# Performance work log

Measured on AMD Instinct MI355X. Metric: run time of the kernel, lower is better.

Reference implementation:

```python
import jax, jax.numpy as jnp
import numpy as np

_SAMPLING_EPS = 1e-5
_NEG_INF = jnp.float32(-jnp.inf)


def setup_inputs() -> dict:
    key = jax.random.key(0)
    k0, k1, k2, k3, k4, k5 = jax.random.split(key, 6)
    T, B, D, V = 4096, 64, 2048, 128000
    hidden_states = jax.random.normal(k0, (T, D), jnp.float32)
    embedding = jax.random.normal(k1, (V, D), jnp.float32) * 0.02
    last_token_indices = jnp.sort(jax.random.randint(k2, (B,), 0, T)).astype(jnp.int64)
    temperatures = jax.random.uniform(k3, (B,), jnp.float32, 0.1, 1.5)
    top_ps = jax.random.uniform(k4, (B,), jnp.float32, 0.5, 1.0)
    top_ks = jax.random.randint(k5, (B,), 1, 1024).astype(jnp.int64)
    return {
        "hidden_states": hidden_states,
        "embedding": embedding,
        "last_token_indices": last_token_indices,
        "temperatures": temperatures,
        "top_ps": top_ps,
        "top_ks": top_ks,
    }


def reference(hidden_states, embedding, last_token_indices, temperatures, top_ps, top_ks):
    V = embedding.shape[0]
    # 1) prune: keep last token of each sequence -> [B, D]
    h = hidden_states[last_token_indices]
    # 2) logits = h @ E^T -> [B, V]
    logits = jnp.einsum("bd,vd->bv", h, embedding)
    # 3) temperature scaling (temp < eps treated as 1.0, greedy handled below)
    t = jnp.where(temperatures < _SAMPLING_EPS, 1.0, temperatures)
    logits = logits / t[:, None]
    # 4) batched top-k in sorted (descending) domain
    sorted_idx = jnp.argsort(-logits, axis=-1)                      # [B, V]
    sorted_logits = jnp.take_along_axis(logits, sorted_idx, axis=-1)
    k = jnp.clip(top_ks, 1, V)
    keep_topk = jnp.arange(V)[None, :] < k[:, None]                  # [B, V]
    sorted_logits = jnp.where(keep_topk, sorted_logits, _NEG_INF)
    # 5) top-p (nucleus) on top-k-filtered, sorted logits
    sorted_probs = jax.nn.softmax(sorted_logits, axis=-1)
    cum = jnp.cumsum(sorted_probs, axis=-1)
    mask_p = (cum > top_ps[:, None]) & (top_ps[:, None] < 1.0 - _SAMPLING_EPS)
    mask_p = mask_p.at[:, 0].set(False)  # always keep the top token
    sorted_logits = jnp.where(mask_p, _NEG_INF, sorted_logits)
    # 6) scatter back to original vocab order
    inv_idx = jnp.argsort(sorted_idx, axis=-1)
    final_logits = jnp.take_along_axis(sorted_logits, inv_idx, axis=-1)
    probs = jax.nn.softmax(final_logits, axis=-1)
    # 7) multinomial sampling via Gumbel-max trick (deterministic key)
    u = jax.random.uniform(jax.random.key(42), probs.shape, jnp.float32, 1e-20, 1.0)
    gumbel = -jnp.log(-jnp.log(u))
    sampled = jnp.argmax(final_logits + gumbel, axis=-1)
    # 8) greedy path when temperature ~ 0
    greedy = jnp.argmax(logits, axis=-1)
    token_ids = jnp.where(temperatures < _SAMPLING_EPS, greedy, sampled)
    # sanitize (clamp out-of-range to 0)
    token_ids = jnp.where((token_ids < 0) | (token_ids >= V), 0, token_ids)
    return token_ids.astype(jnp.int64), probs
```

## Files before the change

kernel.cpp:

```cpp
#include <hip/hip_runtime.h>
#include <hip/hip_bf16.h>
#include <math.h>

#define CAP 2048
#define PRNG_PARTITIONABLE 1

typedef __attribute__((ext_vector_type(8))) short bf16x8;
typedef __attribute__((ext_vector_type(4))) float f32x4;
typedef __attribute__((ext_vector_type(4))) unsigned int u32x4;

union B8U4 { u32x4 u; bf16x8 b; };

#define BARRIER_LDS { asm volatile("s_waitcnt lgkmcnt(0)" ::: "memory"); \
                      __builtin_amdgcn_sched_barrier(0);                  \
                      __builtin_amdgcn_s_barrier(); }

__device__ __forceinline__ unsigned int f2ord(float x) {
  unsigned int u = __float_as_uint(x);
  return (u & 0x80000000u) ? ~u : (u | 0x80000000u);
}

__device__ __forceinline__ unsigned int rotl_u32(unsigned int x, int r) {
  return (x << r) | (x >> (32 - r));
}

__device__ float gumbel_at(unsigned int flat, unsigned int half_n) {
  const unsigned int ks0 = 0u;
  const unsigned int ks1 = 42u;
  const unsigned int ks2 = 0x1BD11BDAu ^ ks0 ^ ks1;
  unsigned int x0, x1;
#if PRNG_PARTITIONABLE
  x0 = 0u;
  x1 = flat;
#else
  unsigned int cnt = (flat < half_n) ? flat : (flat - half_n);
  x0 = cnt; x1 = cnt + half_n;
#endif
  x0 += ks0; x1 += ks1;
#define TF_R(r) { x0 += x1; x1 = rotl_u32(x1, r); x1 ^= x0; }
  TF_R(13) TF_R(15) TF_R(26) TF_R(6)
  x0 += ks1; x1 += ks2 + 1u;
  TF_R(17) TF_R(29) TF_R(16) TF_R(24)
  x0 += ks2; x1 += ks0 + 2u;
  TF_R(13) TF_R(15) TF_R(26) TF_R(6)
  x0 += ks0; x1 += ks1 + 3u;
  TF_R(17) TF_R(29) TF_R(16) TF_R(24)
  x0 += ks1; x1 += ks2 + 4u;
  TF_R(13) TF_R(15) TF_R(26) TF_R(6)
  x0 += ks2; x1 += ks0 + 5u;
#undef TF_R
#if PRNG_PARTITIONABLE
  unsigned int bits = x0 ^ x1;
#else
  unsigned int bits = (flat < half_n) ? x0 : x1;
#endif
  float f = __uint_as_float(0x3f800000u | (bits >> 9)) - 1.0f;
  float u = fmaxf(1e-20f, f + 1e-20f);
  return -logf(-logf(u));
}

__device__ __forceinline__ unsigned short f32_to_bf16_rne(float x) {
  unsigned int u = __float_as_uint(x);
  unsigned int r = u + 0x7fffu + ((u >> 16) & 1u);
  return (unsigned short)(r >> 16);
}
__device__ __forceinline__ float bf16u_to_f32(unsigned short h) {
  return __uint_as_float(((unsigned int)h) << 16);
}

struct HL { unsigned int h, l; };
__device__ __forceinline__ HL cvt_pair(float a, float b) {
  float2 xf = make_float2(a, b);
  __hip_bfloat162 hh = __float22bfloat162_rn(xf);
  float2 hf = __bfloat1622float2(hh);
  __hip_bfloat162 ll = __float22bfloat162_rn(make_float2(a - hf.x, b - hf.y));
  HL r;
  __builtin_memcpy(&r.h, &hh, 4);
  __builtin_memcpy(&r.l, &ll, 4);
  return r;
}

__device__ __forceinline__ f32x4 mfma16(bf16x8 a, bf16x8 b, f32x4 c) {
  return __builtin_amdgcn_mfma_f32_16x16x32_bf16(a, b, c, 0, 0, 0);
}

__global__ void gather_split(const float* __restrict__ hidden, const int* __restrict__ lti,
                             unsigned short* __restrict__ Ah, unsigned short* __restrict__ Al,
                             int D) {
  int b = blockIdx.x;
  const float* src = hidden + (size_t)lti[b] * D;
  for (int i = threadIdx.x; i < D; i += blockDim.x) {
    float x = src[i];
    unsigned short h = f32_to_bf16_rne(x);
    float r = x - bf16u_to_f32(h);
    Ah[(size_t)b * D + i] = h;
    Al[(size_t)b * D + i] = f32_to_bf16_rne(r);
  }
}

#define BN 128
#define BK 64
__global__ __launch_bounds__(256) void gemm_mfma(
    const unsigned short* __restrict__ Ahg, const unsigned short* __restrict__ Alg,
    const float* __restrict__ E, float* __restrict__ outL, int D, int V) {
  __shared__ __align__(16) float BS[128 * 64];
  __shared__ __align__(16) unsigned short AhS[64 * 64];
  __shared__ __align__(16) unsigned short AlS[64 * 64];

  const int t = threadIdx.x;
  const int lane = t & 63;
  const int wv = t >> 6;
  const long n0 = (long)blockIdx.x * BN;
  const int am = t >> 2, ao = t & 3;

  f32x4 acc[4][2];
#pragma unroll
  for (int i = 0; i < 4; ++i)
#pragma unroll
    for (int j = 0; j < 2; ++j) acc[i][j] = (f32x4){0.f, 0.f, 0.f, 0.f};

  f32x4 bA[8], bB[8];
  bf16x8 aA[4], aB[4];

  auto LOAD = [&](f32x4* br, bf16x8* ar, int k0) {
#pragma unroll
    for (int q = 0; q < 4; ++q) {
      int gi = q * 256 + t, n = gi >> 3, o = gi & 7;
      const float* s = E + (size_t)(n0 + n) * D + k0 + o * 8;
      br[2 * q] = *(const f32x4*)s;
      br[2 * q + 1] = *(const f32x4*)(s + 4);
    }
    const unsigned short* ph = Ahg + (size_t)am * D + k0 + ao * 16;
    ar[0] = *(const bf16x8*)ph;
    ar[1] = *(const bf16x8*)(ph + 8);
    const unsigned short* pl = Alg + (size_t)am * D + k0 + ao * 16;
    ar[2] = *(const bf16x8*)pl;
    ar[3] = *(const bf16x8*)(pl + 8);
  };

  auto STAGE = [&](f32x4* br, bf16x8* ar) {
#pragma unroll
    for (int q = 0; q < 4; ++q) {
      int gi = q * 256 + t, n = gi >> 3, o = gi & 7;
      int pg0 = (2 * o) ^ (n & 7);
      int pg1 = (2 * o + 1) ^ (n & 7);
      *(f32x4*)&BS[n * 64 + pg0 * 4] = br[2 * q];
      *(f32x4*)&BS[n * 64 + pg1 * 4] = br[2 * q + 1];
    }
    int g0 = ao * 2;
    int off0 = am * 64 + ((g0 ^ (am & 7)) * 8);
    int off1 = am * 64 + (((g0 + 1) ^ (am & 7)) * 8);
    *(bf16x8*)&AhS[off0] = ar[0];
    *(bf16x8*)&AhS[off1] = ar[1];
    *(bf16x8*)&AlS[off0] = ar[2];
    *(bf16x8*)&AlS[off1] = ar[3];
  };

  auto COMPUTE = [&]() {
#pragma unroll
    for (int k32 = 0; k32 < 2; ++k32) {
      const int og = k32 * 4 + (lane >> 4);
      bf16x8 ah[4], al[4], bh[2], bl[2];
#pragma unroll
      for (int mf = 0; mf < 4; ++mf) {
        int r = mf * 16 + (lane & 15);
        int off = r * 64 + ((og ^ (r & 7)) * 8);
        ah[mf] = *(const bf16x8*)&AhS[off];
        al[mf] = *(const bf16x8*)&AlS[off];
      }
#pragma unroll
      for (int nf = 0; nf < 2; ++nf) {
        int n = wv * 32 + nf * 16 + (lane & 15);
        int pg0 = (2 * og) ^ (n & 7);
        int pg1 = (2 * og + 1) ^ (n & 7);
        f32x4 v0 = *(const f32x4*)&BS[n * 64 + pg0 * 4];
        f32x4 v1 = *(const f32x4*)&BS[n * 64 + pg1 * 4];
        HL p0 = cvt_pair(v0.x, v0.y);
        HL p1 = cvt_pair(v0.z, v0.w);
        HL p2 = cvt_pair(v1.x, v1.y);
        HL p3 = cvt_pair(v1.z, v1.w);
        B8U4 hb, lb;
        hb.u = (u32x4){p0.h, p1.h, p2.h, p3.h};
        lb.u = (u32x4){p0.l, p1.l, p2.l, p3.l};
        bh[nf] = hb.b;
        bl[nf] = lb.b;
      }
      __builtin_amdgcn_s_setprio(1);
#pragma unroll
      for (int mf = 0; mf < 4; ++mf)
#pragma unroll
        for (int nf = 0; nf < 2; ++nf) {
          acc[mf][nf] = mfma16(ah[mf], bh[nf], acc[mf][nf]);
          acc[mf][nf] = mfma16(ah[mf], bl[nf], acc[mf][nf]);
          acc[mf][nf] = mfma16(al[mf], bh[nf], acc[mf][nf]);
        }
      __builtin_amdgcn_s_setprio(0);
    }
  };

  LOAD(bA, aA, 0);
#pragma unroll 1
  for (int k0 = 0; k0 < D; k0 += 2 * BK) {
    if (k0 + BK < D) LOAD(bB, aB, k0 + BK);
    BARRIER_LDS;
    STAGE(bA, aA);
    BARRIER_LDS;
    COMPUTE();
    if (k0 + 2 * BK < D) LOAD(bA, aA, k0 + 2 * BK);
    BARRIER_LDS;
    STAGE(bB, aB);
    BARRIER_LDS;
    COMPUTE();
  }

#pragma unroll
  for (int mf = 0; mf < 4; ++mf)
#pragma unroll
    for (int nf = 0; nf < 2; ++nf) {
      long v = n0 + wv * 32 + nf * 16 + (lane & 15);
      int rbase = mf * 16 + ((lane >> 4) << 2);
#pragma unroll
      for (int reg = 0; reg < 4; ++reg)
        outL[(size_t)(rbase + reg) * V + v] = acc[mf][nf][reg];
    }
}

__global__ __launch_bounds__(256) void hist_k(
    const float* __restrict__ logits, unsigned int* __restrict__ ghist, int V) {
  const int b = blockIdx.x >> 3, c = blockIdx.x & 7;
  const int CH = V >> 3;
  const float* row = logits + (size_t)b * V;
  __shared__ unsigned int lh[4096];
  const int tid = threadIdx.x;
  for (int i = tid; i < 4096; i += 256) lh[i] = 0u;
  __syncthreads();
  const int base = c * CH;
  for (int i = base + tid * 4; i < base + CH; i += 1024) {
    f32x4 v = *(const f32x4*)(row + i);
    atomicAdd(&lh[f2ord(v.x) >> 20], 1u);
    atomicAdd(&lh[f2ord(v.y) >> 20], 1u);
    atomicAdd(&lh[f2ord(v.z) >> 20], 1u);
    atomicAdd(&lh[f2ord(v.w) >> 20], 1u);
  }
  __syncthreads();
  for (int i = tid; i < 4096; i += 256) {
    unsigned int s = lh[i];
    if (s) atomicAdd(&ghist[(size_t)b * 4096 + i], s);
  }
}

__global__ __launch_bounds__(1024) void thresh_k(
    const float* __restrict__ logits, const unsigned int* __restrict__ ghist,
    const int* __restrict__ top_ks, unsigned int* __restrict__ tau20, int V) {
  const int b = blockIdx.x, tid = threadIdx.x;
  __shared__ unsigned int h[4096];
  __shared__ unsigned int ts[1024];
  __shared__ unsigned int h2[256];
  __shared__ int s_bin, s_cntGT, s_found;

  for (int i = tid; i < 4096; i += 1024) h[i] = ghist[(size_t)b * 4096 + i];
  if (tid == 0) s_found = 0;
  __syncthreads();

  int k = top_ks[b];
  if (k < 1) k = 1;
  if (k > V) k = V;
  const unsigned int uk = (unsigned int)k;

  unsigned int s0 = h[4 * tid] + h[4 * tid + 1] + h[4 * tid + 2] + h[4 * tid + 3];
  ts[tid] = s0;
  __syncthreads();
  for (int off = 1; off < 1024; off <<= 1) {
    unsigned int v = ts[tid] + ((tid + off < 1024) ? ts[tid + off] : 0u);
    __syncthreads();
    ts[tid] = v;
    __syncthreads();
  }
  unsigned int above = ts[tid] - s0;
  if (above < uk && above + s0 >= uk) {
    unsigned int run = above;
    for (int j = 3; j >= 0; --j) {
      unsigned int hj = h[4 * tid + j];
      if (run < uk && run + hj >= uk) {
        s_bin = 4 * tid + j;
        s_cntGT = (int)run;
        s_found = 1;
        break;
      }
      run += hj;
    }
  }
  __syncthreads();
  int bin = s_found ? s_bin : 0;
  int cntGT = s_found ? s_cntGT : 0;

  if (cntGT + (int)h[bin] <= CAP) {
    if (tid == 0) tau20[b] = ((unsigned int)bin) << 8;
    return;
  }

  for (int i = tid; i < 256; i += 1024) h2[i] = 0u;
  __syncthreads();
  const float* row = logits + (size_t)b * V;
  const unsigned int binq = (unsigned int)bin;
  for (int i = tid * 4; i < V; i += 4096) {
    f32x4 v = *(const f32x4*)(row + i);
#pragma unroll
    for (int e = 0; e < 4; ++e) {
      unsigned int u = f2ord(v[e]);
      if ((u >> 20) == binq) atomicAdd(&h2[(u >> 12) & 255u], 1u);
    }
  }
  __syncthreads();
  if (tid == 0) {
    int need = k - cntGT;
    unsigned int run = 0;
    int sub = 255;
    for (; sub >= 0; --sub) {
      unsigned int hh = h2[sub];
      if (run + hh >= (unsigned int)need) break;
      run += hh;
    }
    if (sub < 0) sub = 0;
    tau20[b] = (binq << 8) | (unsigned int)sub;
  }
}

__global__ __launch_bounds__(256) void gather_k(
    float* __restrict__ logits, const unsigned int* __restrict__ tau20,
    float* __restrict__ cvals, int* __restrict__ cidx, int* __restrict__ ccnt, int V) {
  const int b = blockIdx.x >> 3, c = blockIdx.x & 7;
  const int CH = V >> 3;
  float* row = logits + (size_t)b * V;
  __shared__ float bv[CAP];
  __shared__ int bi[CAP];
  __shared__ int s_c, s_base;
  const int tid = threadIdx.x;
  if (tid == 0) s_c = 0;
  __syncthreads();
  const unsigned int tau = tau20[b];
  const int base = c * CH;
  const f32x4 z = (f32x4){0.f, 0.f, 0.f, 0.f};
  for (int i = base + tid * 4; i < base + CH; i += 1024) {
    f32x4 v = *(const f32x4*)(row + i);
#pragma unroll
    for (int e = 0; e < 4; ++e) {
      float x = v[e];
      if ((f2ord(x) >> 12) >= tau) {
        int p = atomicAdd(&s_c, 1);
        if (p < CAP) { bv[p] = x; bi[p] = i + e; }
      }
    }
    *(f32x4*)(row + i) = z;
  }
  __syncthreads();
  int cnt = s_c;
  if (cnt > CAP) cnt = CAP;
  if (tid == 0) s_base = atomicAdd(ccnt + b, cnt);
  __syncthreads();
  const int gb = s_base;
  for (int i = tid; i < cnt; i += 256) {
    int p = gb + i;
    if (p < CAP) {
      cvals[(size_t)b * CAP + p] = bv[i];
      cidx[(size_t)b * CAP + p] = bi[i];
    }
  }
}

__global__ __launch_bounds__(1024) void finalize_k(
    const float* __restrict__ cvals, const int* __restrict__ cidx,
    const int* __restrict__ ccnt, const int* __restrict__ top_ks,
    const float* __restrict__ temps, const float* __restrict__ top_ps,
    float* __restrict__ out, int probs_base, int V, unsigned int half_n) {
  const int b = blockIdx.x, tid = threadIdx.x;
  __shared__ float vals[CAP];
  __shared__ int idxs[CAP];
  __shared__ float ex[1024];
  __shared__ float pr[1024];
  __shared__ float rsc[1024];
  __shared__ int rid[1024];
  __shared__ float s_S, s_S2;
  __shared__ int s_m;

  int cnt = ccnt[b];
  if (cnt > CAP) cnt = CAP;
  int k = top_ks[b];
  if (k < 1) k = 1;
  if (k > V) k = V;
  int K = (k < cnt) ? k : cnt;
  if (K > 1024) K = 1024;

  for (int i = tid; i < CAP; i += 1024) {
    if (i < cnt) { vals[i] = cvals[(size_t)b * CAP + i]; idxs[i] = cidx[(size_t)b * CAP + i]; }
    else         { vals[i] = -INFINITY;                  idxs[i] = 0x7fffffff; }
  }
  __syncthreads();

  for (int size = 2; size <= CAP; size <<= 1) {
    for (int stride = size >> 1; stride > 0; stride >>= 1) {
      for (int i = tid; i < CAP; i += 1024) {
        int j = i ^ stride;
        if (j > i) {
          float vi = vals[i], vj = vals[j];
          int ii = idxs[i], ij = idxs[j];
          bool iBeforeJ = (vi > vj) || (vi == vj && ii < ij);
          bool up = ((i & size) == 0);
          if (up ? !iBeforeJ : iBeforeJ) {
            vals[i] = vj; idxs[i] = ij; vals[j] = vi; idxs[j] = ii;
          }
        }
      }
      __syncthreads();
    }
  }

  const float t = temps[b];
  const float tt = (t < 1e-5f) ? 1.0f : t;
  const float l0 = vals[0] / tt;
  ex[tid] = (tid < K) ? expf(vals[tid] / tt - l0) : 0.f;
  __syncthreads();

  rsc[tid] = ex[tid];
  __syncthreads();
  for (int s = 512; s > 0; s >>= 1) {
    if (tid < s) rsc[tid] += rsc[tid + s];
    __syncthreads();
  }
  if (tid == 0) s_S = rsc[0];
  __syncthreads();
  const float S = s_S;

  const float p = top_ps[b];
  int m;
  if (p >= 1.0f - 1e-5f) {
    m = K;
  } else {
    pr[tid] = ex[tid] / S;
    __syncthreads();
    for (int off = 1; off < 1024; off <<= 1) {
      float v = pr[tid] + ((tid >= off) ? pr[tid - off] : 0.f);
      __syncthreads();
      pr[tid] = v;
      __syncthreads();
    }
    rid[tid] = (tid < K && pr[tid] <= p) ? 1 : 0;
    __syncthreads();
    for (int s = 512; s > 0; s >>= 1) {
      if (tid < s) rid[tid] += rid[tid + s];
      __syncthreads();
    }
    if (tid == 0) s_m = (rid[0] < 1) ? 1 : rid[0];
    __syncthreads();
    m = s_m;
  }
  __syncthreads();

  rsc[tid] = (tid < m) ? ex[tid] : 0.f;
  __syncthreads();
  for (int s = 512; s > 0; s >>= 1) {
    if (tid < s) rsc[tid] += rsc[tid + s];
    __syncthreads();
  }
  if (tid == 0) s_S2 = rsc[0];
  __syncthreads();
  const float S2 = s_S2;

  for (int i = tid; i < m; i += 1024)
    out[(size_t)probs_base + (size_t)b * V + idxs[i]] = ex[i] / S2;

  float best = -INFINITY;
  int bestV = 0x7fffffff;
  for (int i = tid; i < m; i += 1024) {
    int vv = idxs[i];
    unsigned int flat = (unsigned int)b * (unsigned int)V + (unsigned int)vv;
    float g = gumbel_at(flat, half_n);
    float sc = vals[i] / tt + g;
    if (sc > best || (sc == best && vv < bestV)) { best = sc; bestV = vv; }
  }
  rsc[tid] = best; rid[tid] = bestV;
  __syncthreads();
  for (int s = 512; s > 0; s >>= 1) {
    if (tid < s) {
      float o = rsc[tid + s]; int oi = rid[tid + s];
      if (o > rsc[tid] || (o == rsc[tid] && oi < rid[tid])) { rsc[tid] = o; rid[tid] = oi; }
    }
    __syncthreads();
  }
  if (tid == 0) {
    int token = (t < 1e-5f) ? idxs[0] : rid[0];
    if (token < 0 || token >= V) token = 0;
    out[b] = (float)token;
  }
}

extern "C" void kernel_launch(void* const* d_in, const int* in_sizes, int n_in,
                              void* d_out, int out_size, void* d_ws, size_t ws_size,
                              hipStream_t stream) {
  const float* hidden = (const float*)d_in[0];
  const float* emb    = (const float*)d_in[1];
  const int*   lti    = (const int*)d_in[2];
  const float* temps  = (const float*)d_in[3];
  const float* tops   = (const float*)d_in[4];
  const int*   topks  = (const int*)d_in[5];

  const int B = in_sizes[2];
  const int V = (int)(((long long)out_size - B) / B);
  const int D = in_sizes[1] / V;
  const int probs_base = out_size - B * V;
  const unsigned int half_n = (unsigned int)(((long long)B * V) / 2);

  float* out = (float*)d_out;

  char* ws = (char*)d_ws;
  size_t off = 0;
  unsigned short* Ah = (unsigned short*)(ws + off); off += (size_t)B * D * sizeof(unsigned short);
  unsigned short* Al = (unsigned short*)(ws + off); off += (size_t)B * D * sizeof(unsigned short);
  float* cvals = (float*)(ws + off); off += (size_t)B * CAP * sizeof(float);
  int* cidx = (int*)(ws + off);      off += (size_t)B * CAP * sizeof(int);
  char* zbase = ws + off;
  int* ccnt = (int*)(ws + off);                    off += (size_t)B * sizeof(int);
  unsigned int* ghist = (unsigned int*)(ws + off); off += (size_t)B * 4096 * sizeof(unsigned int);
  const size_t zbytes = (size_t)(B + B * 4096) * sizeof(unsigned int);
  unsigned int* tau20 = (unsigned int*)(ws + off); off += (size_t)B * sizeof(unsigned int);
  (void)ws_size; (void)n_in;

  float* logits = out + probs_base;

  hipLaunchKernelGGL(gather_split, dim3(B), dim3(256), 0, stream, hidden, lti, Ah, Al, D);
  hipMemsetAsync(zbase, 0, zbytes, stream);
  hipLaunchKernelGGL(gemm_mfma, dim3(V / BN), dim3(256), 0, stream, Ah, Al, emb, logits, D, V);
  hipLaunchKernelGGL(hist_k, dim3(8 * B), dim3(256), 0, stream, logits, ghist, V);
  hipLaunchKernelGGL(thresh_k, dim3(B), dim3(1024), 0, stream, logits, ghist, topks, tau20, V);
  hipLaunchKernelGGL(gather_k, dim3(8 * B), dim3(256), 0, stream, logits, tau20, cvals, cidx, ccnt, V);
  hipLaunchKernelGGL(finalize_k, dim3(B), dim3(1024), 0, stream, cvals, cidx, ccnt,
                     topks, temps, tops, out, probs_base, V, half_n);
}
```

Before: 329.9 us.

## Merge histogram, threshold and gather into one cooperative kernel with grid syncs

Replaces the three top-k selection kernels and the workspace memset with a single cooperative launch that uses grid-wide syncs between the histogram, threshold and gather phases. Per-chunk histograms go to separate slices written with plain stores instead of global atomics, so no zeroing memset is needed, and ccnt is reset inside the kernel. The goal is to remove launch gaps and the memset. In exchange, the threshold phase now runs on one 256-thread block per row instead of a 1024-thread block, and the two grid barriers add their own cost.

```diff
diff --git a/kernel.cpp b/kernel.cpp
--- a/kernel.cpp
+++ b/kernel.cpp
@@ -1,6 +1,9 @@
 #include <hip/hip_runtime.h>
 #include <hip/hip_bf16.h>
+#include <hip/hip_cooperative_groups.h>
 #include <math.h>
+
+namespace cg = cooperative_groups;
 
 #define CAP 2048
 #define PRNG_PARTITIONABLE 1
@@ -225,145 +228,153 @@
     }
 }
 
-__global__ __launch_bounds__(256) void hist_k(
-    const float* __restrict__ logits, unsigned int* __restrict__ ghist, int V) {
+__global__ __launch_bounds__(256) void select_coop(
+    float* __restrict__ logits, const int* __restrict__ top_ks,
+    unsigned int* __restrict__ gslices, unsigned int* __restrict__ tau20,
+    float* __restrict__ cvals, int* __restrict__ cidx, int* __restrict__ ccnt,
+    int V) {
+  cg::grid_group grid = cg::this_grid();
+  const int tid = threadIdx.x;
   const int b = blockIdx.x >> 3, c = blockIdx.x & 7;
   const int CH = V >> 3;
-  const float* row = logits + (size_t)b * V;
-  __shared__ unsigned int lh[4096];
-  const int tid = threadIdx.x;
-  for (int i = tid; i < 4096; i += 256) lh[i] = 0u;
-  __syncthreads();
-  const int base = c * CH;
-  for (int i = base + tid * 4; i < base + CH; i += 1024) {
-    f32x4 v = *(const f32x4*)(row + i);
-    atomicAdd(&lh[f2ord(v.x) >> 20], 1u);
-    atomicAdd(&lh[f2ord(v.y) >> 20], 1u);
-    atomicAdd(&lh[f2ord(v.z) >> 20], 1u);
-    atomicAdd(&lh[f2ord(v.w) >> 20], 1u);
-  }
-  __syncthreads();
-  for (int i = tid; i < 4096; i += 256) {
-    unsigned int s = lh[i];
-    if (s) atomicAdd(&ghist[(size_t)b * 4096 + i], s);
-  }
-}
-
-__global__ __launch_bounds__(1024) void thresh_k(
-    const float* __restrict__ logits, const unsigned int* __restrict__ ghist,
-    const int* __restrict__ top_ks, unsigned int* __restrict__ tau20, int V) {
-  const int b = blockIdx.x, tid = threadIdx.x;
-  __shared__ unsigned int h[4096];
-  __shared__ unsigned int ts[1024];
+
+  __shared__ unsigned int sh[4096];
+  __shared__ unsigned int ts[256];
   __shared__ unsigned int h2[256];
-  __shared__ int s_bin, s_cntGT, s_found;
-
-  for (int i = tid; i < 4096; i += 1024) h[i] = ghist[(size_t)b * 4096 + i];
-  if (tid == 0) s_found = 0;
-  __syncthreads();
-
-  int k = top_ks[b];
-  if (k < 1) k = 1;
-  if (k > V) k = V;
-  const unsigned int uk = (unsigned int)k;
-
-  unsigned int s0 = h[4 * tid] + h[4 * tid + 1] + h[4 * tid + 2] + h[4 * tid + 3];
-  ts[tid] = s0;
-  __syncthreads();
-  for (int off = 1; off < 1024; off <<= 1) {
-    unsigned int v = ts[tid] + ((tid + off < 1024) ? ts[tid + off] : 0u);
-    __syncthreads();
-    ts[tid] = v;
-    __syncthreads();
-  }
-  unsigned int above = ts[tid] - s0;
-  if (above < uk && above + s0 >= uk) {
-    unsigned int run = above;
-    for (int j = 3; j >= 0; --j) {
-      unsigned int hj = h[4 * tid + j];
-      if (run < uk && run + hj >= uk) {
-        s_bin = 4 * tid + j;
-        s_cntGT = (int)run;
-        s_found = 1;
-        break;
-      }
-      run += hj;
-    }
-  }
-  __syncthreads();
-  int bin = s_found ? s_bin : 0;
-  int cntGT = s_found ? s_cntGT : 0;
-
-  if (cntGT + (int)h[bin] <= CAP) {
-    if (tid == 0) tau20[b] = ((unsigned int)bin) << 8;
-    return;
-  }
-
-  for (int i = tid; i < 256; i += 1024) h2[i] = 0u;
-  __syncthreads();
-  const float* row = logits + (size_t)b * V;
-  const unsigned int binq = (unsigned int)bin;
-  for (int i = tid * 4; i < V; i += 4096) {
-    f32x4 v = *(const f32x4*)(row + i);
-#pragma unroll
-    for (int e = 0; e < 4; ++e) {
-      unsigned int u = f2ord(v[e]);
-      if ((u >> 20) == binq) atomicAdd(&h2[(u >> 12) & 255u], 1u);
-    }
-  }
-  __syncthreads();
-  if (tid == 0) {
-    int need = k - cntGT;
-    unsigned int run = 0;
-    int sub = 255;
-    for (; sub >= 0; --sub) {
-      unsigned int hh = h2[sub];
-      if (run + hh >= (unsigned int)need) break;
-      run += hh;
-    }
-    if (sub < 0) sub = 0;
-    tau20[b] = (binq << 8) | (unsigned int)sub;
-  }
-}
-
-__global__ __launch_bounds__(256) void gather_k(
-    float* __restrict__ logits, const unsigned int* __restrict__ tau20,
-    float* __restrict__ cvals, int* __restrict__ cidx, int* __restrict__ ccnt, int V) {
-  const int b = blockIdx.x >> 3, c = blockIdx.x & 7;
-  const int CH = V >> 3;
+  __shared__ int s_bin, s_cntGT, s_found, s_c, s_base;
+
   float* row = logits + (size_t)b * V;
-  __shared__ float bv[CAP];
-  __shared__ int bi[CAP];
-  __shared__ int s_c, s_base;
-  const int tid = threadIdx.x;
-  if (tid == 0) s_c = 0;
-  __syncthreads();
-  const unsigned int tau = tau20[b];
-  const int base = c * CH;
-  const f32x4 z = (f32x4){0.f, 0.f, 0.f, 0.f};
-  for (int i = base + tid * 4; i < base + CH; i += 1024) {
-    f32x4 v = *(const f32x4*)(row + i);
-#pragma unroll
-    for (int e = 0; e < 4; ++e) {
-      float x = v[e];
-      if ((f2ord(x) >> 12) >= tau) {
-        int p = atomicAdd(&s_c, 1);
-        if (p < CAP) { bv[p] = x; bi[p] = i + e; }
-      }
-    }
-    *(f32x4*)(row + i) = z;
-  }
-  __syncthreads();
-  int cnt = s_c;
-  if (cnt > CAP) cnt = CAP;
-  if (tid == 0) s_base = atomicAdd(ccnt + b, cnt);
-  __syncthreads();
-  const int gb = s_base;
-  for (int i = tid; i < cnt; i += 256) {
-    int p = gb + i;
-    if (p < CAP) {
-      cvals[(size_t)b * CAP + p] = bv[i];
-      cidx[(size_t)b * CAP + p] = bi[i];
+
+  for (int i = tid; i < 4096; i += 256) sh[i] = 0u;
+  __syncthreads();
+  {
+    const int base = c * CH;
+    for (int i = base + tid * 4; i < base + CH; i += 1024) {
+      f32x4 v = *(const f32x4*)(row + i);
+      atomicAdd(&sh[f2ord(v.x) >> 20], 1u);
+      atomicAdd(&sh[f2ord(v.y) >> 20], 1u);
+      atomicAdd(&sh[f2ord(v.z) >> 20], 1u);
+      atomicAdd(&sh[f2ord(v.w) >> 20], 1u);
+    }
+  }
+  __syncthreads();
+  {
+    unsigned int* slice = gslices + ((size_t)b * 8 + c) * 4096;
+    for (int i = tid; i < 4096; i += 256) slice[i] = sh[i];
+  }
+
+  grid.sync();
+
+  if (c == 0) {
+    const unsigned int* sl = gslices + (size_t)b * 8 * 4096;
+    for (int i = tid; i < 4096; i += 256) {
+      unsigned int s = 0;
+#pragma unroll
+      for (int cc = 0; cc < 8; ++cc) s += sl[cc * 4096 + i];
+      sh[i] = s;
+    }
+    if (tid == 0) s_found = 0;
+    __syncthreads();
+
+    int k = top_ks[b];
+    if (k < 1) k = 1;
+    if (k > V) k = V;
+    const unsigned int uk = (unsigned int)k;
+
+    unsigned int s0 = 0;
+#pragma unroll
+    for (int j = 0; j < 16; ++j) s0 += sh[16 * tid + j];
+    ts[tid] = s0;
+    __syncthreads();
+    for (int off = 1; off < 256; off <<= 1) {
+      unsigned int v = ts[tid] + ((tid + off < 256) ? ts[tid + off] : 0u);
+      __syncthreads();
+      ts[tid] = v;
+      __syncthreads();
+    }
+    unsigned int above = ts[tid] - s0;
+    if (above < uk && above + s0 >= uk) {
+      unsigned int run = above;
+      for (int j = 15; j >= 0; --j) {
+        unsigned int hj = sh[16 * tid + j];
+        if (run < uk && run + hj >= uk) {
+          s_bin = 16 * tid + j;
+          s_cntGT = (int)run;
+          s_found = 1;
+          break;
+        }
+        run += hj;
+      }
+    }
+    __syncthreads();
+    int bin = s_found ? s_bin : 0;
+    int cntGT = s_found ? s_cntGT : 0;
+
+    if (cntGT + (int)sh[bin] <= CAP) {
+      if (tid == 0) { tau20[b] = ((unsigned int)bin) << 8; ccnt[b] = 0; }
+    } else {
+      for (int i = tid; i < 256; i += 256) h2[i] = 0u;
+      __syncthreads();
+      const unsigned int binq = (unsigned int)bin;
+      for (int i = tid * 4; i < V; i += 1024) {
+        f32x4 v = *(const f32x4*)(row + i);
+#pragma unroll
+        for (int e = 0; e < 4; ++e) {
+          unsigned int u = f2ord(v[e]);
+          if ((u >> 20) == binq) atomicAdd(&h2[(u >> 12) & 255u], 1u);
+        }
+      }
+      __syncthreads();
+      if (tid == 0) {
+        int need = k - cntGT;
+        unsigned int run = 0;
+        int sub = 255;
+        for (; sub >= 0; --sub) {
+          unsigned int hh = h2[sub];
+          if (run + hh >= (unsigned int)need) break;
+          run += hh;
+        }
+        if (sub < 0) sub = 0;
+        tau20[b] = (binq << 8) | (unsigned int)sub;
+        ccnt[b] = 0;
+      }
+    }
+  }
+
+  grid.sync();
+
+  {
+    float* bv = (float*)sh;
+    int* bi = (int*)(sh + CAP);
+    if (tid == 0) s_c = 0;
+    __syncthreads();
+    const unsigned int tau = tau20[b];
+    const int base = c * CH;
+    const f32x4 z = (f32x4){0.f, 0.f, 0.f, 0.f};
+    for (int i = base + tid * 4; i < base + CH; i += 1024) {
+      f32x4 v = *(const f32x4*)(row + i);
+#pragma unroll
+      for (int e = 0; e < 4; ++e) {
+        float x = v[e];
+        if ((f2ord(x) >> 12) >= tau) {
+          int p = atomicAdd(&s_c, 1);
+          if (p < CAP) { bv[p] = x; bi[p] = i + e; }
+        }
+      }
+      *(f32x4*)(row + i) = z;
+    }
+    __syncthreads();
+    int cnt = s_c;
+    if (cnt > CAP) cnt = CAP;
+    if (tid == 0) s_base = atomicAdd(ccnt + b, cnt);
+    __syncthreads();
+    const int gb = s_base;
+    for (int i = tid; i < cnt; i += 256) {
+      int p = gb + i;
+      if (p < CAP) {
+        cvals[(size_t)b * CAP + p] = bv[i];
+        cidx[(size_t)b * CAP + p] = bi[i];
+      }
     }
   }
 }
@@ -518,21 +529,22 @@
   unsigned short* Al = (unsigned short*)(ws + off); off += (size_t)B * D * sizeof(unsigned short);
   float* cvals = (float*)(ws + off); off += (size_t)B * CAP * sizeof(float);
   int* cidx = (int*)(ws + off);      off += (size_t)B * CAP * sizeof(int);
-  char* zbase = ws + off;
-  int* ccnt = (int*)(ws + off);                    off += (size_t)B * sizeof(int);
-  unsigned int* ghist = (unsigned int*)(ws + off); off += (size_t)B * 4096 * sizeof(unsigned int);
-  const size_t zbytes = (size_t)(B + B * 4096) * sizeof(unsigned int);
-  unsigned int* tau20 = (unsigned int*)(ws + off); off += (size_t)B * sizeof(unsigned int);
+  int* ccnt = (int*)(ws + off);      off += (size_t)B * sizeof(int);
+  unsigned int* gslices = (unsigned int*)(ws + off); off += (size_t)B * 8 * 4096 * sizeof(unsigned int);
+  unsigned int* tau20 = (unsigned int*)(ws + off);   off += (size_t)B * sizeof(unsigned int);
   (void)ws_size; (void)n_in;
 
   float* logits = out + probs_base;
 
   hipLaunchKernelGGL(gather_split, dim3(B), dim3(256), 0, stream, hidden, lti, Ah, Al, D);
-  hipMemsetAsync(zbase, 0, zbytes, stream);
   hipLaunchKernelGGL(gemm_mfma, dim3(V / BN), dim3(256), 0, stream, Ah, Al, emb, logits, D, V);
-  hipLaunchKernelGGL(hist_k, dim3(8 * B), dim3(256), 0, stream, logits, ghist, V);
-  hipLaunchKernelGGL(thresh_k, dim3(B), dim3(1024), 0, stream, logits, ghist, topks, tau20, V);
-  hipLaunchKernelGGL(gather_k, dim3(8 * B), dim3(256), 0, stream, logits, tau20, cvals, cidx, ccnt, V);
+  {
+    int Vv = V;
+    void* args[] = {(void*)&logits, (void*)&topks, (void*)&gslices, (void*)&tau20,
+                    (void*)&cvals, (void*)&cidx, (void*)&ccnt, (void*)&Vv};
+    hipLaunchCooperativeKernel((const void*)select_coop, dim3(8 * B), dim3(256),
+                               args, 0, stream);
+  }
   hipLaunchKernelGGL(finalize_k, dim3(B), dim3(1024), 0, stream, cvals, cidx, ccnt,
                      topks, temps, tops, out, probs_base, V, half_n);
 }
```

Result: slower. 452.2 us (+37.1%).
